# Kernel optimization log

Measured on AMD Instinct MI355X. Metric: run time of the kernel, lower is better.

## Reference

```python
import jax, jax.numpy as jnp
import numpy as np

N_NODES = 50000
N_EDGES = 1600000
HIDDEN = 128
N_RBF = 50


def _linear_init(key, fan_in, fan_out):
    # mimic torch nn.Linear default init: U(-1/sqrt(fan_in), 1/sqrt(fan_in))
    kw, kb = jax.random.split(key)
    bound = 1.0 / np.sqrt(fan_in)
    W = jax.random.uniform(kw, (fan_in, fan_out), minval=-bound, maxval=bound, dtype=jnp.float32)
    b = jax.random.uniform(kb, (fan_out,), minval=-bound, maxval=bound, dtype=jnp.float32)
    return W, b


def setup_inputs() -> dict:
    key = jax.random.key(0)
    ks = jax.random.split(key, 9)
    x = jax.random.normal(ks[0], (N_NODES, HIDDEN), dtype=jnp.float32)
    edge_index = jax.random.randint(ks[1], (2, N_EDGES), 0, N_NODES, dtype=jnp.int32)
    edge_attr = jax.random.uniform(ks[2], (N_EDGES, N_RBF), dtype=jnp.float32)
    fW1, fb1 = _linear_init(ks[3], N_RBF, HIDDEN)
    fW2, fb2 = _linear_init(ks[4], HIDDEN, HIDDEN)
    dW, db = _linear_init(ks[5], HIDDEN, HIDDEN)
    uW1, ub1 = _linear_init(ks[6], HIDDEN, HIDDEN)
    uW2, ub2 = _linear_init(ks[7], HIDDEN, HIDDEN)
    return {
        "x": x, "edge_index": edge_index, "edge_attr": edge_attr,
        "fW1": fW1, "fb1": fb1, "fW2": fW2, "fb2": fb2,
        "dW": dW, "db": db,
        "uW1": uW1, "ub1": ub1, "uW2": uW2, "ub2": ub2,
    }


def reference(x, edge_index, edge_attr, fW1, fb1, fW2, fb2, dW, db, uW1, ub1, uW2, ub2):
    src, dst = edge_index[0], edge_index[1]
    # filter network: Linear -> SiLU -> Linear on edge RBF features [E, n_rbf] -> [E, H]
    filters = jax.nn.silu(edge_attr @ fW1 + fb1) @ fW2 + fb2
    # messages: dense(x[src]) * filters  [E, H]
    messages = (x[src] @ dW + db) * filters
    # scatter-add to destination nodes
    aggregated = jax.ops.segment_sum(messages, dst, num_segments=x.shape[0])
    # update MLP + residual
    upd = jax.nn.silu(aggregated @ uW1 + ub1) @ uW2 + ub2
    return x + upd
```

## Files before the change

kernel.cpp:

```cpp
#include <hip/hip_runtime.h>

#define H    128
#define RBF  50
#define K1   64
#define EB   64
#define NB   32
#define NBLK 1024

typedef _Float16 f16;
typedef _Float16 f16x2 __attribute__((ext_vector_type(2)));
typedef _Float16 f16x4 __attribute__((ext_vector_type(4)));
typedef _Float16 f16x8 __attribute__((ext_vector_type(8)));
typedef float    f32x4 __attribute__((ext_vector_type(4)));

#define HS_LD 136

__device__ __forceinline__ float silu_f(float a) {
    return a / (1.0f + __expf(-a));
}


__global__ __launch_bounds__(256) void hist_kernel(
    const int* __restrict__ dst, int* __restrict__ counts, int E)
{
    for (int i = blockIdx.x * 256 + threadIdx.x; i < E; i += gridDim.x * 256)
        atomicAdd(&counts[dst[i]], 1);
}

__global__ __launch_bounds__(256) void scan1_kernel(
    const int* __restrict__ counts, int* __restrict__ ofs, int* __restrict__ bsum, int N)
{
    __shared__ int s[256];
    const int t = threadIdx.x;
    const int g = blockIdx.x * 256 + t;
    int v = (g < N) ? counts[g] : 0;
    s[t] = v; __syncthreads();
    for (int off = 1; off < 256; off <<= 1) {
        int u = 0; if (t >= off) u = s[t - off];
        __syncthreads(); s[t] += u; __syncthreads();
    }
    if (g < N) ofs[g] = s[t] - v;
    if (t == 255) bsum[blockIdx.x] = s[255];
}
__global__ __launch_bounds__(256) void scan2_kernel(int* __restrict__ bsum, int nb)
{
    __shared__ int s[256];
    const int t = threadIdx.x;
    int v = (t < nb) ? bsum[t] : 0;
    s[t] = v; __syncthreads();
    for (int off = 1; off < 256; off <<= 1) {
        int u = 0; if (t >= off) u = s[t - off];
        __syncthreads(); s[t] += u; __syncthreads();
    }
    if (t < nb) bsum[t] = s[t] - v;
}
__global__ __launch_bounds__(256) void scan3_kernel(
    int* __restrict__ ofs, const int* __restrict__ bsum, int N)
{
    int g = blockIdx.x * 256 + threadIdx.x;
    if (g < N) ofs[g] += bsum[blockIdx.x];
}

__global__ __launch_bounds__(256) void ranges_kernel(
    const int* __restrict__ ofs, int* __restrict__ nstart, int* __restrict__ estart,
    int N, int E, int B)
{
    int b = blockIdx.x * 256 + threadIdx.x;
    if (b > B) return;
    if (b == B) { nstart[B] = N; estart[B] = E; return; }
    long long cb = (long long)b * E / B;
    int lo = 0, hi = N;
    while (lo < hi) {
        int mid = (lo + hi) >> 1;
        int val = (mid < N) ? ofs[mid] : E;
        if (val < (int)cb) lo = mid + 1; else hi = mid;
    }
    nstart[b] = lo;
    estart[b] = (lo < N) ? ofs[lo] : E;
}

__global__ __launch_bounds__(256) void scatter_rec_kernel(
    const int* __restrict__ src, const int* __restrict__ dst,
    int* __restrict__ cursor, int4* __restrict__ rec, int E)
{
    for (int i = blockIdx.x * 256 + threadIdx.x; i < E; i += gridDim.x * 256) {
        int d = dst[i];
        int pos = atomicAdd(&cursor[d], 1);
        rec[pos] = make_int4(i, src[i], d, 0);
    }
}


__global__ __launch_bounds__(256) void convert_weights_kernel(
    const float* __restrict__ fW1, const float* __restrict__ fW2,
    f16* __restrict__ Wt1, f16* __restrict__ Wt2)
{
    int i = blockIdx.x * 256 + threadIdx.x;
    if (i < H * K1) {
        int n = i >> 6, k = i & (K1 - 1);
        Wt1[i] = (k < RBF) ? (f16)fW1[k * H + n] : (f16)0.f;
    }
    int j = i - H * K1;
    if (j >= 0 && j < H * H) {
        int n = j >> 7, k = j & (H - 1);
        Wt2[j] = (f16)fW2[k * H + n];
    }
}

__global__ __launch_bounds__(256) void compute_h_kernel(
    const float* __restrict__ x, const float* __restrict__ dW,
    const float* __restrict__ db, f16* __restrict__ h, int N)
{
    __shared__ float xs[NB][H];
    const int tid = threadIdx.x;
    const int n0  = blockIdx.x * NB;
    for (int idx = tid; idx < NB * H; idx += 256) {
        int r = idx >> 7, c = idx & (H - 1);
        int n = n0 + r;
        xs[r][c] = (n < N) ? x[(size_t)n * H + c] : 0.f;
    }
    __syncthreads();
    const int j  = tid & (H - 1);
    const int rb = (tid >> 7) * 16;
    float acc[16];
    const float b = db[j];
#pragma unroll
    for (int r = 0; r < 16; ++r) acc[r] = b;
    for (int kq = 0; kq < H / 4; ++kq) {
        const int k = kq * 4;
        const float w0 = dW[(k + 0) * H + j];
        const float w1 = dW[(k + 1) * H + j];
        const float w2 = dW[(k + 2) * H + j];
        const float w3 = dW[(k + 3) * H + j];
#pragma unroll
        for (int r = 0; r < 16; ++r) {
            const float4 v = *(const float4*)&xs[rb + r][k];
            acc[r] = fmaf(v.x, w0, fmaf(v.y, w1, fmaf(v.z, w2, fmaf(v.w, w3, acc[r]))));
        }
    }
#pragma unroll
    for (int r = 0; r < 16; ++r) {
        int n = n0 + rb + r;
        if (n < N) h[(size_t)n * H + j] = (f16)acc[r];
    }
}

__device__ __forceinline__ void ea_frag_write(
    f16* uni, int j, int s,
    const float4& f0, const float4& f1, const float4& f2, const float2& f3)
{
    char* base = (char*)uni;
    {
        f16x4 v; v[0]=(f16)f0.x; v[1]=(f16)f0.y; v[2]=(f16)f0.z; v[3]=(f16)f0.w;
        *(f16x4*)(base + (size_t)(((0 + (s >> 1)) * 64 + j) * 16 + (s & 1) * 8)) = v;
    }
    {
        f16x4 v; v[0]=(f16)f1.x; v[1]=(f16)f1.y; v[2]=(f16)f1.z; v[3]=(f16)f1.w;
        *(f16x4*)(base + (size_t)(((2 + (s >> 1)) * 64 + j) * 16 + (s & 1) * 8)) = v;
    }
    {
        f16x4 v; v[0]=(f16)f2.x; v[1]=(f16)f2.y; v[2]=(f16)f2.z; v[3]=(f16)f2.w;
        *(f16x4*)(base + (size_t)(((4 + (s >> 1)) * 64 + j) * 16 + (s & 1) * 8)) = v;
    }
    if (s == 0) {
        char* b6 = base + (size_t)((6 * 64 + j) * 16);
        f16x2 v2; v2[0]=(f16)f3.x; v2[1]=(f16)f3.y;
        f16x2 z2 = {};
        *(f16x2*)(b6)      = v2;
        *(f16x2*)(b6 + 4)  = z2;
        *(f16x2*)(b6 + 8)  = z2;
        *(f16x2*)(b6 + 12) = z2;
    } else if (s == 1) {
        f16x8 z8 = {};
        *(f16x8*)(base + (size_t)((7 * 64 + j) * 16)) = z8;
    }
}

__global__ __launch_bounds__(256, 4) void edge_fused_kernel(
    const float* __restrict__ ea, const int4* __restrict__ rec,
    const f16* __restrict__ Wt1, const f16* __restrict__ Wt2,
    const float* __restrict__ fb1, const float* __restrict__ fb2,
    const f16* __restrict__ h, float* __restrict__ out,
    const int* __restrict__ nstart, const int* __restrict__ estart)
{
    __shared__ __align__(16) f16 uni[8192];
    __shared__ __align__(16) f16 h_s[EB * HS_LD];
    __shared__ int dst_s[EB];

    const int tid  = threadIdx.x;
    const int lane = tid & 63;
    const int wv   = tid >> 6;
    const int wr   = (wv >> 1) * 32;
    const int wc   = (wv & 1) * 64;
    const int fr   = lane & 15;
    const int qw   = lane >> 4;
    const int kb   = qw * 8;

    const int j = tid >> 2;
    const int s = tid & 3;

    f16x8 B1[4][2];
    f16x8 B2[4][4];
    float b1v[4], b2v[4];
#pragma unroll
    for (int ct = 0; ct < 4; ++ct) {
        const int col = wc + ct * 16 + fr;
#pragma unroll
        for (int ks = 0; ks < 2; ++ks)
            B1[ct][ks] = *(const f16x8*)&Wt1[col * K1 + ks * 32 + kb];
#pragma unroll
        for (int ks = 0; ks < 4; ++ks)
            B2[ct][ks] = *(const f16x8*)&Wt2[col * H + ks * 32 + kb];
        b1v[ct] = fb1[col];
        b2v[ct] = fb2[col];
    }

    const int ns = nstart[blockIdx.x], ne = nstart[blockIdx.x + 1];
    const int e0 = estart[blockIdx.x], e1 = estart[blockIdx.x + 1];

    if (e0 >= e1) {
        for (int idx = tid; idx < (ne - ns) * H; idx += 256)
            out[(size_t)ns * H + idx] = 0.f;
        return;
    }

    const int col128 = tid & 127;
    int   curdst = ns;
    float accv   = 0.f;

    int4 recP;
    {
        int idx = e0 + j; idx = (idx < e1) ? idx : (e1 - 1);
        recP = rec[idx];
    }

    for (int tb = e0; tb < e1; tb += EB) {
        int4 recN;
        {
            int idx = tb + EB + j; idx = (idx < e1) ? idx : (e1 - 1);
            recN = rec[idx];
        }

        {
            const f16* hp = h + (size_t)recP.y * H + s * 8;
            const f16x8 h0 = *(const f16x8*)(hp);
            const f16x8 h1 = *(const f16x8*)(hp + 32);
            const f16x8 h2 = *(const f16x8*)(hp + 64);
            const f16x8 h3 = *(const f16x8*)(hp + 96);
            const float* ep = ea + (size_t)recP.x * RBF + s * 4;
            const float4 ef0 = *(const float4*)(ep);
            const float4 ef1 = *(const float4*)(ep + 16);
            const float4 ef2 = *(const float4*)(ep + 32);
            float2 ef3 = {};
            if (s == 0) ef3 = *(const float2*)(ea + (size_t)recP.x * RBF + 48);

            *(f16x8*)&h_s[j * HS_LD +  0 + s * 8] = h0;
            *(f16x8*)&h_s[j * HS_LD + 32 + s * 8] = h1;
            *(f16x8*)&h_s[j * HS_LD + 64 + s * 8] = h2;
            *(f16x8*)&h_s[j * HS_LD + 96 + s * 8] = h3;
            ea_frag_write(uni, j, s, ef0, ef1, ef2, ef3);
            if (s == 0) dst_s[j] = (tb + j < e1) ? recP.z : ne;
        }
        __syncthreads();

        f32x4 acc1[2][4];
#pragma unroll
        for (int rt = 0; rt < 2; ++rt)
#pragma unroll
            for (int ct = 0; ct < 4; ++ct)
                acc1[rt][ct] = (f32x4){b1v[ct], b1v[ct], b1v[ct], b1v[ct]};
#pragma unroll
        for (int ks = 0; ks < 2; ++ks) {
            const f16x8 A0 = *(const f16x8*)((char*)uni + (size_t)(((ks * 4 + qw) * 64 + wr + fr) * 16));
            const f16x8 A1 = *(const f16x8*)((char*)uni + (size_t)(((ks * 4 + qw) * 64 + wr + 16 + fr) * 16));
#pragma unroll
            for (int ct = 0; ct < 4; ++ct) {
                acc1[0][ct] = __builtin_amdgcn_mfma_f32_16x16x32_f16(A0, B1[ct][ks], acc1[0][ct], 0, 0, 0);
                acc1[1][ct] = __builtin_amdgcn_mfma_f32_16x16x32_f16(A1, B1[ct][ks], acc1[1][ct], 0, 0, 0);
            }
        }
        __syncthreads();

#pragma unroll
        for (int rt = 0; rt < 2; ++rt)
#pragma unroll
            for (int ct = 0; ct < 4; ++ct)
#pragma unroll
                for (int m = 0; m < 4; ++m) {
                    const int er = wr + rt * 16 + qw * 4 + m;
                    const int c  = wc + ct * 16 + fr;
                    *(f16*)((char*)uni + (size_t)(((c >> 3) * 64 + er) * 16 + (c & 7) * 2)) =
                        (f16)silu_f(acc1[rt][ct][m]);
                }
        __syncthreads();

        f32x4 acc2[2][4];
#pragma unroll
        for (int rt = 0; rt < 2; ++rt)
#pragma unroll
            for (int ct = 0; ct < 4; ++ct)
                acc2[rt][ct] = (f32x4){b2v[ct], b2v[ct], b2v[ct], b2v[ct]};
#pragma unroll
        for (int ks = 0; ks < 4; ++ks) {
            const f16x8 A0 = *(const f16x8*)((char*)uni + (size_t)(((ks * 4 + qw) * 64 + wr + fr) * 16));
            const f16x8 A1 = *(const f16x8*)((char*)uni + (size_t)(((ks * 4 + qw) * 64 + wr + 16 + fr) * 16));
#pragma unroll
            for (int ct = 0; ct < 4; ++ct) {
                acc2[0][ct] = __builtin_amdgcn_mfma_f32_16x16x32_f16(A0, B2[ct][ks], acc2[0][ct], 0, 0, 0);
                acc2[1][ct] = __builtin_amdgcn_mfma_f32_16x16x32_f16(A1, B2[ct][ks], acc2[1][ct], 0, 0, 0);
            }
        }

#pragma unroll
        for (int rt = 0; rt < 2; ++rt)
#pragma unroll
            for (int ct = 0; ct < 4; ++ct)
#pragma unroll
                for (int m = 0; m < 4; ++m) {
                    const int er = wr + rt * 16 + qw * 4 + m;
                    const int c  = wc + ct * 16 + fr;
                    f16* p = &h_s[er * HS_LD + c];
                    *p = (f16)((float)*p * acc2[rt][ct][m]);
                }
        __syncthreads();

        if (tid < 128) {
            for (int r = 0; r < EB; ++r) {
                const int d = dst_s[r];
                const float v = (float)h_s[r * HS_LD + col128];
                if (d != curdst) {
                    out[(size_t)curdst * H + col128] = accv;
                    for (int n = curdst + 1; n < d; ++n) out[(size_t)n * H + col128] = 0.f;
                    curdst = d; accv = 0.f;
                }
                if (d < ne) accv += v;
            }
        }
        __syncthreads();

        recP = recN;
    }

    if (tid < 128 && curdst < ne) {
        out[(size_t)curdst * H + col128] = accv;
        for (int n = curdst + 1; n < ne; ++n) out[(size_t)n * H + col128] = 0.f;
    }
}

__global__ __launch_bounds__(256) void update_kernel(
    const float* __restrict__ x,
    const float* __restrict__ uW1, const float* __restrict__ ub1,
    const float* __restrict__ uW2, const float* __restrict__ ub2,
    float* __restrict__ out, int N)
{
    __shared__ float as[NB][H];
    __shared__ float ts[NB][H];
    const int tid = threadIdx.x;
    const int n0  = blockIdx.x * NB;
    for (int idx = tid; idx < NB * H; idx += 256) {
        int r = idx >> 7, c = idx & (H - 1);
        int n = n0 + r;
        as[r][c] = (n < N) ? out[(size_t)n * H + c] : 0.f;
    }
    __syncthreads();
    const int j  = tid & (H - 1);
    const int rb = (tid >> 7) * 16;
    float acc[16];
    {
        const float b1 = ub1[j];
#pragma unroll
        for (int r = 0; r < 16; ++r) acc[r] = b1;
    }
    for (int kq = 0; kq < H / 4; ++kq) {
        const int k = kq * 4;
        const float w0 = uW1[(k + 0) * H + j];
        const float w1 = uW1[(k + 1) * H + j];
        const float w2 = uW1[(k + 2) * H + j];
        const float w3 = uW1[(k + 3) * H + j];
#pragma unroll
        for (int r = 0; r < 16; ++r) {
            const float4 v = *(const float4*)&as[rb + r][k];
            acc[r] = fmaf(v.x, w0, fmaf(v.y, w1, fmaf(v.z, w2, fmaf(v.w, w3, acc[r]))));
        }
    }
#pragma unroll
    for (int r = 0; r < 16; ++r) ts[rb + r][j] = silu_f(acc[r]);
    __syncthreads();
    {
        const float b2 = ub2[j];
#pragma unroll
        for (int r = 0; r < 16; ++r) acc[r] = b2;
    }
    for (int kq = 0; kq < H / 4; ++kq) {
        const int k = kq * 4;
        const float w0 = uW2[(k + 0) * H + j];
        const float w1 = uW2[(k + 1) * H + j];
        const float w2 = uW2[(k + 2) * H + j];
        const float w3 = uW2[(k + 3) * H + j];
#pragma unroll
        for (int r = 0; r < 16; ++r) {
            const float4 v = *(const float4*)&ts[rb + r][k];
            acc[r] = fmaf(v.x, w0, fmaf(v.y, w1, fmaf(v.z, w2, fmaf(v.w, w3, acc[r]))));
        }
    }
#pragma unroll
    for (int r = 0; r < 16; ++r) {
        int n = n0 + rb + r;
        if (n < N) out[(size_t)n * H + j] = x[(size_t)n * H + j] + acc[r];
    }
}

extern "C" void kernel_launch(void* const* d_in, const int* in_sizes, int n_in,
                              void* d_out, int out_size, void* d_ws, size_t ws_size,
                              hipStream_t stream) {
    const float* x   = (const float*)d_in[0];
    const int*   ei  = (const int*)  d_in[1];
    const float* ea  = (const float*)d_in[2];
    const float* fW1 = (const float*)d_in[3];
    const float* fb1 = (const float*)d_in[4];
    const float* fW2 = (const float*)d_in[5];
    const float* fb2 = (const float*)d_in[6];
    const float* dW  = (const float*)d_in[7];
    const float* db  = (const float*)d_in[8];
    const float* uW1 = (const float*)d_in[9];
    const float* ub1 = (const float*)d_in[10];
    const float* uW2 = (const float*)d_in[11];
    const float* ub2 = (const float*)d_in[12];

    float* out = (float*)d_out;
    const int N = in_sizes[0] / H;
    const int E = in_sizes[1] / 2;
    const int* src = ei;
    const int* dst = ei + E;

    char* ws = (char*)d_ws;
    size_t off = 0;
    auto alloc = [&](size_t bytes) { void* p = ws + off; off = (off + bytes + 255) & ~(size_t)255; return p; };
    f16*  h      = (f16*) alloc((size_t)N * H * sizeof(f16));
    f16*  Wt1    = (f16*) alloc((size_t)H * K1 * sizeof(f16));
    f16*  Wt2    = (f16*) alloc((size_t)H * H * sizeof(f16));
    int*  counts = (int*) alloc((size_t)N * sizeof(int));
    int*  ofs    = (int*) alloc((size_t)N * sizeof(int));
    int*  bsum   = (int*) alloc(256 * sizeof(int));
    int*  nstart = (int*) alloc((size_t)(NBLK + 1) * sizeof(int));
    int*  estart = (int*) alloc((size_t)(NBLK + 1) * sizeof(int));
    int4* rec    = (int4*)alloc((size_t)E * sizeof(int4));

    const int nscan = (N + 255) / 256;

    hipMemsetAsync(counts, 0, (size_t)N * sizeof(int), stream);
    convert_weights_kernel<<<(H * K1 + H * H + 255) / 256, 256, 0, stream>>>(fW1, fW2, Wt1, Wt2);
    compute_h_kernel<<<(N + NB - 1) / NB, 256, 0, stream>>>(x, dW, db, h, N);

    hist_kernel<<<2048, 256, 0, stream>>>(dst, counts, E);
    scan1_kernel<<<nscan, 256, 0, stream>>>(counts, ofs, bsum, N);
    scan2_kernel<<<1, 256, 0, stream>>>(bsum, nscan);
    scan3_kernel<<<nscan, 256, 0, stream>>>(ofs, bsum, N);

    ranges_kernel<<<(NBLK + 256) / 256, 256, 0, stream>>>(ofs, nstart, estart, N, E, NBLK);
    scatter_rec_kernel<<<2048, 256, 0, stream>>>(src, dst, ofs, rec, E);

    edge_fused_kernel<<<NBLK, 256, 0, stream>>>(
        ea, rec, Wt1, Wt2, fb1, fb2, h, out, nstart, estart);

    update_kernel<<<(N + NB - 1) / NB, 256, 0, stream>>>(
        x, uW1, ub1, uW2, ub2, out, N);
}
```

Before: 926.4 us.

## Double-buffer gathered node rows and overlap segment reduction with next tile

Gathers x[src] rows straight into LDS with global_load_lds into a double-buffered, XOR-swizzled tile. The scatter reduction of the previous tile now runs while the next tile's loads are in flight, which removes one barrier per iteration. LDS use roughly doubles, so occupancy drops to 3 blocks per CU and the block count falls to 768. The swizzle replaces the padded row stride to avoid bank conflicts. The risks are lower occupancy and ordering hazards between the async LDS loads and the barriers.

```diff
diff --git a/kernel.cpp b/kernel.cpp
--- a/kernel.cpp
+++ b/kernel.cpp
@@ -5,7 +5,7 @@
 #define K1   64
 #define EB   64
 #define NB   32
-#define NBLK 1024
+#define NBLK 768
 
 typedef _Float16 f16;
 typedef _Float16 f16x2 __attribute__((ext_vector_type(2)));
@@ -13,10 +13,21 @@
 typedef _Float16 f16x8 __attribute__((ext_vector_type(8)));
 typedef float    f32x4 __attribute__((ext_vector_type(4)));
 
-#define HS_LD 136
+#define SWZH(R) ((((R) >> 1) & 7) << 4)
 
 __device__ __forceinline__ float silu_f(float a) {
     return a / (1.0f + __expf(-a));
+}
+
+__device__ __forceinline__ void gl2lds16(const f16* g, f16* l) {
+#if defined(__has_builtin) && __has_builtin(__builtin_amdgcn_global_load_lds)
+    __builtin_amdgcn_global_load_lds(
+        (const __attribute__((address_space(1))) void*)g,
+        (__attribute__((address_space(3))) void*)l, 16, 0, 0);
+#else
+    const int lane = threadIdx.x & 63;
+    *(f16x8*)(l + lane * 8) = *(const f16x8*)g;
+#endif
 }
 
 
@@ -176,7 +187,7 @@
     }
 }
 
-__global__ __launch_bounds__(256, 4) void edge_fused_kernel(
+__global__ __launch_bounds__(256, 3) void edge_fused_kernel(
     const float* __restrict__ ea, const int4* __restrict__ rec,
     const f16* __restrict__ Wt1, const f16* __restrict__ Wt2,
     const float* __restrict__ fb1, const float* __restrict__ fb2,
@@ -184,8 +195,8 @@
     const int* __restrict__ nstart, const int* __restrict__ estart)
 {
     __shared__ __align__(16) f16 uni[8192];
-    __shared__ __align__(16) f16 h_s[EB * HS_LD];
-    __shared__ int dst_s[EB];
+    __shared__ __align__(16) f16 h_s[2][8192];
+    __shared__ int dst_s[2][EB];
 
     const int tid  = threadIdx.x;
     const int lane = tid & 63;
@@ -227,39 +238,49 @@
     const int col128 = tid & 127;
     int   curdst = ns;
     float accv   = 0.f;
+    int   cur    = 0;
 
     int4 recP;
-    {
-        int idx = e0 + j; idx = (idx < e1) ? idx : (e1 - 1);
-        recP = rec[idx];
-    }
+    { int idx = e0 + j; idx = (idx < e1) ? idx : (e1 - 1); recP = rec[idx]; }
 
     for (int tb = e0; tb < e1; tb += EB) {
-        int4 recN;
         {
-            int idx = tb + EB + j; idx = (idx < e1) ? idx : (e1 - 1);
-            recN = rec[idx];
+            const int recPy = recP.y;
+#pragma unroll
+            for (int i = 0; i < 4; ++i) {
+                const int R  = wv * 16 + i * 4 + (lane >> 4);
+                const int sy = __shfl(recPy, (i * 4 + (lane >> 4)) * 4, 64);
+                const f16* g = h + (size_t)sy * H + ((((lane & 15) * 16) ^ SWZH(R)) >> 1);
+                gl2lds16(g, &h_s[cur][wv * 2048 + i * 512]);
+            }
         }
 
         {
-            const f16* hp = h + (size_t)recP.y * H + s * 8;
-            const f16x8 h0 = *(const f16x8*)(hp);
-            const f16x8 h1 = *(const f16x8*)(hp + 32);
-            const f16x8 h2 = *(const f16x8*)(hp + 64);
-            const f16x8 h3 = *(const f16x8*)(hp + 96);
             const float* ep = ea + (size_t)recP.x * RBF + s * 4;
             const float4 ef0 = *(const float4*)(ep);
             const float4 ef1 = *(const float4*)(ep + 16);
             const float4 ef2 = *(const float4*)(ep + 32);
             float2 ef3 = {};
             if (s == 0) ef3 = *(const float2*)(ea + (size_t)recP.x * RBF + 48);
-
-            *(f16x8*)&h_s[j * HS_LD +  0 + s * 8] = h0;
-            *(f16x8*)&h_s[j * HS_LD + 32 + s * 8] = h1;
-            *(f16x8*)&h_s[j * HS_LD + 64 + s * 8] = h2;
-            *(f16x8*)&h_s[j * HS_LD + 96 + s * 8] = h3;
             ea_frag_write(uni, j, s, ef0, ef1, ef2, ef3);
-            if (s == 0) dst_s[j] = (tb + j < e1) ? recP.z : ne;
+            if (s == 0) dst_s[cur][j] = (tb + j < e1) ? recP.z : ne;
+        }
+
+        int4 recN;
+        { int idx = tb + EB + j; idx = (idx < e1) ? idx : (e1 - 1); recN = rec[idx]; }
+
+        if (tb > e0 && tid < 128) {
+            const int pb = cur ^ 1;
+            for (int r = 0; r < EB; ++r) {
+                const int d = dst_s[pb][r];
+                const float v = (float)h_s[pb][(r * 256 + ((col128 * 2) ^ SWZH(r))) >> 1];
+                if (d != curdst) {
+                    out[(size_t)curdst * H + col128] = accv;
+                    for (int n = curdst + 1; n < d; ++n) out[(size_t)n * H + col128] = 0.f;
+                    curdst = d; accv = 0.f;
+                }
+                if (d < ne) accv += v;
+            }
         }
         __syncthreads();
 
@@ -319,31 +340,30 @@
                 for (int m = 0; m < 4; ++m) {
                     const int er = wr + rt * 16 + qw * 4 + m;
                     const int c  = wc + ct * 16 + fr;
-                    f16* p = &h_s[er * HS_LD + c];
+                    f16* p = &h_s[cur][(er * 256 + ((c * 2) ^ SWZH(er))) >> 1];
                     *p = (f16)((float)*p * acc2[rt][ct][m]);
                 }
         __syncthreads();
 
-        if (tid < 128) {
-            for (int r = 0; r < EB; ++r) {
-                const int d = dst_s[r];
-                const float v = (float)h_s[r * HS_LD + col128];
-                if (d != curdst) {
-                    out[(size_t)curdst * H + col128] = accv;
-                    for (int n = curdst + 1; n < d; ++n) out[(size_t)n * H + col128] = 0.f;
-                    curdst = d; accv = 0.f;
-                }
-                if (d < ne) accv += v;
+        recP = recN; cur ^= 1;
+    }
+
+    if (tid < 128) {
+        const int pb = cur ^ 1;
+        for (int r = 0; r < EB; ++r) {
+            const int d = dst_s[pb][r];
+            const float v = (float)h_s[pb][(r * 256 + ((col128 * 2) ^ SWZH(r))) >> 1];
+            if (d != curdst) {
+                out[(size_t)curdst * H + col128] = accv;
+                for (int n = curdst + 1; n < d; ++n) out[(size_t)n * H + col128] = 0.f;
+                curdst = d; accv = 0.f;
             }
-        }
-        __syncthreads();
-
-        recP = recN;
-    }
-
-    if (tid < 128 && curdst < ne) {
-        out[(size_t)curdst * H + col128] = accv;
-        for (int n = curdst + 1; n < ne; ++n) out[(size_t)n * H + col128] = 0.f;
+            if (d < ne) accv += v;
+        }
+        if (curdst < ne) {
+            out[(size_t)curdst * H + col128] = accv;
+            for (int n = curdst + 1; n < ne; ++n) out[(size_t)n * H + col128] = 0.f;
+        }
     }
 }
 
```

Result: slower. 1.063 ms (+14.7%).

## Pre-permute edge features into dst-sorted fp16 padded layout before fused edge kernel

Applied to the files above, without the earlier changes.

Adds a permute pass that reads edge_attr coalesced in original order, converts it to fp16 padded to 64 columns, and writes it in dst-sorted order. The fused edge kernel can then stream its edge features contiguously instead of gathering scattered fp32 rows. The sort record shrinks from int4 to int2 (src,dst), and a separate cursor array stops the scatter from clobbering the offsets. This adds an extra pass that reads 320MB and writes about 200MB, plus a rank array, in exchange for a cheaper and more regular load inside the main edge kernel.

```diff
diff --git a/kernel.cpp b/kernel.cpp
--- a/kernel.cpp
+++ b/kernel.cpp
@@ -8,7 +8,6 @@
 #define NBLK 1024
 
 typedef _Float16 f16;
-typedef _Float16 f16x2 __attribute__((ext_vector_type(2)));
 typedef _Float16 f16x4 __attribute__((ext_vector_type(4)));
 typedef _Float16 f16x8 __attribute__((ext_vector_type(8)));
 typedef float    f32x4 __attribute__((ext_vector_type(4)));
@@ -55,10 +54,14 @@
     if (t < nb) bsum[t] = s[t] - v;
 }
 __global__ __launch_bounds__(256) void scan3_kernel(
-    int* __restrict__ ofs, const int* __restrict__ bsum, int N)
+    int* __restrict__ ofs, int* __restrict__ cursor, const int* __restrict__ bsum, int N)
 {
     int g = blockIdx.x * 256 + threadIdx.x;
-    if (g < N) ofs[g] += bsum[blockIdx.x];
+    if (g < N) {
+        int v = ofs[g] + bsum[blockIdx.x];
+        ofs[g] = v;
+        cursor[g] = v;
+    }
 }
 
 __global__ __launch_bounds__(256) void ranges_kernel(
@@ -79,15 +82,48 @@
     estart[b] = (lo < N) ? ofs[lo] : E;
 }
 
-__global__ __launch_bounds__(256) void scatter_rec_kernel(
+__global__ __launch_bounds__(256) void scatter_kernel(
     const int* __restrict__ src, const int* __restrict__ dst,
-    int* __restrict__ cursor, int4* __restrict__ rec, int E)
+    int* __restrict__ cursor, int* __restrict__ rank, int2* __restrict__ sd, int E)
 {
     for (int i = blockIdx.x * 256 + threadIdx.x; i < E; i += gridDim.x * 256) {
         int d = dst[i];
         int pos = atomicAdd(&cursor[d], 1);
-        rec[pos] = make_int4(i, src[i], d, 0);
-    }
+        rank[i] = pos;
+        sd[pos] = make_int2(src[i], d);
+    }
+}
+
+__global__ __launch_bounds__(256) void permute_ea_kernel(
+    const float* __restrict__ ea, const int* __restrict__ rank,
+    f16* __restrict__ ea16, int E)
+{
+    const int tid = threadIdx.x;
+    const int e = blockIdx.x * EB + (tid >> 2);
+    const int s = tid & 3;
+    if (e >= E) return;
+    const int p = rank[e];
+    const float* rp = ea + (size_t)e * RBF;
+
+    const float4 a = *(const float4*)(rp + s * 8);
+    const float4 b = *(const float4*)(rp + s * 8 + 4);
+    float4 c4 = {}, d4 = {};
+    if (s < 2) {
+        c4 = *(const float4*)(rp + 32 + s * 8);
+        d4 = *(const float4*)(rp + 36 + s * 8);
+    } else if (s == 2) {
+        const float2 t2 = *(const float2*)(rp + 48);
+        c4.x = t2.x; c4.y = t2.y;
+    }
+    f16x8 v1, v2;
+    v1[0]=(f16)a.x; v1[1]=(f16)a.y; v1[2]=(f16)a.z; v1[3]=(f16)a.w;
+    v1[4]=(f16)b.x; v1[5]=(f16)b.y; v1[6]=(f16)b.z; v1[7]=(f16)b.w;
+    v2[0]=(f16)c4.x; v2[1]=(f16)c4.y; v2[2]=(f16)c4.z; v2[3]=(f16)c4.w;
+    v2[4]=(f16)d4.x; v2[5]=(f16)d4.y; v2[6]=(f16)d4.z; v2[7]=(f16)d4.w;
+
+    f16* op = ea16 + (size_t)p * K1;
+    *(f16x8*)(op + s * 8)      = v1;
+    *(f16x8*)(op + 32 + s * 8) = v2;
 }
 
 
@@ -145,43 +181,12 @@
     }
 }
 
-__device__ __forceinline__ void ea_frag_write(
-    f16* uni, int j, int s,
-    const float4& f0, const float4& f1, const float4& f2, const float2& f3)
-{
-    char* base = (char*)uni;
-    {
-        f16x4 v; v[0]=(f16)f0.x; v[1]=(f16)f0.y; v[2]=(f16)f0.z; v[3]=(f16)f0.w;
-        *(f16x4*)(base + (size_t)(((0 + (s >> 1)) * 64 + j) * 16 + (s & 1) * 8)) = v;
-    }
-    {
-        f16x4 v; v[0]=(f16)f1.x; v[1]=(f16)f1.y; v[2]=(f16)f1.z; v[3]=(f16)f1.w;
-        *(f16x4*)(base + (size_t)(((2 + (s >> 1)) * 64 + j) * 16 + (s & 1) * 8)) = v;
-    }
-    {
-        f16x4 v; v[0]=(f16)f2.x; v[1]=(f16)f2.y; v[2]=(f16)f2.z; v[3]=(f16)f2.w;
-        *(f16x4*)(base + (size_t)(((4 + (s >> 1)) * 64 + j) * 16 + (s & 1) * 8)) = v;
-    }
-    if (s == 0) {
-        char* b6 = base + (size_t)((6 * 64 + j) * 16);
-        f16x2 v2; v2[0]=(f16)f3.x; v2[1]=(f16)f3.y;
-        f16x2 z2 = {};
-        *(f16x2*)(b6)      = v2;
-        *(f16x2*)(b6 + 4)  = z2;
-        *(f16x2*)(b6 + 8)  = z2;
-        *(f16x2*)(b6 + 12) = z2;
-    } else if (s == 1) {
-        f16x8 z8 = {};
-        *(f16x8*)(base + (size_t)((7 * 64 + j) * 16)) = z8;
-    }
-}
-
 __global__ __launch_bounds__(256, 4) void edge_fused_kernel(
-    const float* __restrict__ ea, const int4* __restrict__ rec,
+    const f16* __restrict__ ea16, const int2* __restrict__ sd,
     const f16* __restrict__ Wt1, const f16* __restrict__ Wt2,
     const float* __restrict__ fb1, const float* __restrict__ fb2,
     const f16* __restrict__ h, float* __restrict__ out,
-    const int* __restrict__ nstart, const int* __restrict__ estart)
+    const int* __restrict__ nstart, const int* __restrict__ estart, int E)
 {
     __shared__ __align__(16) f16 uni[8192];
     __shared__ __align__(16) f16 h_s[EB * HS_LD];
@@ -228,38 +233,32 @@
     int   curdst = ns;
     float accv   = 0.f;
 
-    int4 recP;
-    {
-        int idx = e0 + j; idx = (idx < e1) ? idx : (e1 - 1);
-        recP = rec[idx];
-    }
+    int2 sdP;
+    { int idx = e0 + j; idx = (idx < e1) ? idx : (e1 - 1); sdP = sd[idx]; }
 
     for (int tb = e0; tb < e1; tb += EB) {
-        int4 recN;
+        int2 sdN;
+        { int idx = tb + EB + j; idx = (idx < e1) ? idx : (e1 - 1); sdN = sd[idx]; }
+
         {
-            int idx = tb + EB + j; idx = (idx < e1) ? idx : (e1 - 1);
-            recN = rec[idx];
-        }
-
-        {
-            const f16* hp = h + (size_t)recP.y * H + s * 8;
+            const f16* hp = h + (size_t)sdP.x * H + s * 8;
             const f16x8 h0 = *(const f16x8*)(hp);
             const f16x8 h1 = *(const f16x8*)(hp + 32);
             const f16x8 h2 = *(const f16x8*)(hp + 64);
             const f16x8 h3 = *(const f16x8*)(hp + 96);
-            const float* ep = ea + (size_t)recP.x * RBF + s * 4;
-            const float4 ef0 = *(const float4*)(ep);
-            const float4 ef1 = *(const float4*)(ep + 16);
-            const float4 ef2 = *(const float4*)(ep + 32);
-            float2 ef3 = {};
-            if (s == 0) ef3 = *(const float2*)(ea + (size_t)recP.x * RBF + 48);
+
+            const int pe = tb + j;
+            const f16* ep = ea16 + (size_t)((pe < E) ? pe : (E - 1)) * K1;
+            const f16x8 ev1 = *(const f16x8*)(ep + s * 8);
+            const f16x8 ev2 = *(const f16x8*)(ep + 32 + s * 8);
 
             *(f16x8*)&h_s[j * HS_LD +  0 + s * 8] = h0;
             *(f16x8*)&h_s[j * HS_LD + 32 + s * 8] = h1;
             *(f16x8*)&h_s[j * HS_LD + 64 + s * 8] = h2;
             *(f16x8*)&h_s[j * HS_LD + 96 + s * 8] = h3;
-            ea_frag_write(uni, j, s, ef0, ef1, ef2, ef3);
-            if (s == 0) dst_s[j] = (tb + j < e1) ? recP.z : ne;
+            *(f16x8*)((char*)uni + (size_t)(((s)     * 64 + j) * 16)) = ev1;
+            *(f16x8*)((char*)uni + (size_t)(((4 + s) * 64 + j) * 16)) = ev2;
+            if (s == 0) dst_s[j] = (pe < e1) ? sdP.y : ne;
         }
         __syncthreads();
 
@@ -338,7 +337,7 @@
         }
         __syncthreads();
 
-        recP = recN;
+        sdP = sdN;
     }
 
     if (tid < 128 && curdst < ne) {
@@ -441,12 +440,16 @@
     f16*  Wt2    = (f16*) alloc((size_t)H * H * sizeof(f16));
     int*  counts = (int*) alloc((size_t)N * sizeof(int));
     int*  ofs    = (int*) alloc((size_t)N * sizeof(int));
+    int*  cursor = (int*) alloc((size_t)N * sizeof(int));
     int*  bsum   = (int*) alloc(256 * sizeof(int));
     int*  nstart = (int*) alloc((size_t)(NBLK + 1) * sizeof(int));
     int*  estart = (int*) alloc((size_t)(NBLK + 1) * sizeof(int));
-    int4* rec    = (int4*)alloc((size_t)E * sizeof(int4));
-
-    const int nscan = (N + 255) / 256;
+    int*  rank   = (int*) alloc((size_t)E * sizeof(int));
+    int2* sd     = (int2*)alloc((size_t)E * sizeof(int2));
+    f16*  ea16   = (f16*) alloc((size_t)E * K1 * sizeof(f16));
+
+    const int nscan  = (N + 255) / 256;
+    const int ntiles = (E + EB - 1) / EB;
 
     hipMemsetAsync(counts, 0, (size_t)N * sizeof(int), stream);
     convert_weights_kernel<<<(H * K1 + H * H + 255) / 256, 256, 0, stream>>>(fW1, fW2, Wt1, Wt2);
@@ -455,13 +458,14 @@
     hist_kernel<<<2048, 256, 0, stream>>>(dst, counts, E);
     scan1_kernel<<<nscan, 256, 0, stream>>>(counts, ofs, bsum, N);
     scan2_kernel<<<1, 256, 0, stream>>>(bsum, nscan);
-    scan3_kernel<<<nscan, 256, 0, stream>>>(ofs, bsum, N);
+    scan3_kernel<<<nscan, 256, 0, stream>>>(ofs, cursor, bsum, N);
 
     ranges_kernel<<<(NBLK + 256) / 256, 256, 0, stream>>>(ofs, nstart, estart, N, E, NBLK);
-    scatter_rec_kernel<<<2048, 256, 0, stream>>>(src, dst, ofs, rec, E);
+    scatter_kernel<<<2048, 256, 0, stream>>>(src, dst, cursor, rank, sd, E);
+    permute_ea_kernel<<<ntiles, 256, 0, stream>>>(ea, rank, ea16, E);
 
     edge_fused_kernel<<<NBLK, 256, 0, stream>>>(
-        ea, rec, Wt1, Wt2, fb1, fb2, h, out, nstart, estart);
+        ea16, sd, Wt1, Wt2, fb1, fb2, h, out, nstart, estart, E);
 
     update_kernel<<<(N + NB - 1) / NB, 256, 0, stream>>>(
         x, uW1, ub1, uW2, ub2, out, N);
```

New measurement: 947.3 us. +2.3%, slower.
